# Performance work log

Hardware: AMD Instinct MI355X
Metric: run time of the kernel (lower is better)

## Reference

```python
import jax, jax.numpy as jnp
import numpy as np

GRID_H = GRID_W = 17
IMG_H = IMG_W = 128
HFOV = 60.0
ZNEAR, ZFAR = 1.0, 100.0          # FoVPerspectiveCameras defaults
Z_EPS = 0.01                      # MeshRasterizerWithZClamp.z_eps
BLUR_RADIUS = 1e-4
K_FACES = 8                       # faces_per_pixel
SIGMA = 1e-4
GAMMA = 1e-4
BG_COLOR = np.array([0.0, 0.0, 0.0], dtype=np.float32)
Z_BACKGROUND = 100.0


def _build_faces(H, W):
    # Exact replication of the 8 list comprehensions in NovelViewProjector.__init__ (flip=False)
    idx = lambda y, x: y * W + x
    f = []
    for ny in range(0, H - 1, 2):
        for nx in range(1, W - 1, 2):
            f.append([idx(ny, nx + 1), idx(ny, nx), idx(ny + 1, nx)])
    for ny in range(0, H - 1, 2):
        for nx in range(1, W - 1, 2):
            f.append([idx(ny, nx + 1), idx(ny + 1, nx), idx(ny + 1, nx + 1)])
    for ny in range(0, H - 1, 2):
        for nx in range(0, W - 1, 2):
            f.append([idx(ny, nx + 1), idx(ny, nx), idx(ny + 1, nx + 1)])
    for ny in range(0, H - 1, 2):
        for nx in range(0, W - 1, 2):
            f.append([idx(ny + 1, nx + 1), idx(ny, nx), idx(ny + 1, nx)])
    for ny in range(1, H - 1, 2):
        for nx in range(0, W - 1, 2):
            f.append([idx(ny, nx + 1), idx(ny, nx), idx(ny + 1, nx)])
    for ny in range(1, H - 1, 2):
        for nx in range(0, W - 1, 2):
            f.append([idx(ny, nx + 1), idx(ny + 1, nx), idx(ny + 1, nx + 1)])
    for ny in range(1, H - 1, 2):
        for nx in range(1, W - 1, 2):
            f.append([idx(ny, nx + 1), idx(ny, nx), idx(ny + 1, nx + 1)])
    for ny in range(1, H - 1, 2):
        for nx in range(1, W - 1, 2):
            f.append([idx(ny + 1, nx + 1), idx(ny, nx), idx(ny + 1, nx)])
    return np.array(f, dtype=np.int32)


_FACES = _build_faces(GRID_H, GRID_W)                                   # [F,3]
_xs_uv = np.linspace(1, 0, GRID_W)
_ys_uv = np.linspace(0, 1, GRID_H)
_VERTS_UVS = np.array([[x, y] for y in _ys_uv for x in _xs_uv], np.float32)  # [V,2]
_xs = np.linspace(-1, 1, GRID_W)
_ys = np.linspace(-1, 1, GRID_H)
_UNSCALED_GRID = np.array([[x, y] for y in _ys for x in _xs], np.float32)   # [V,2]
_SCALE = np.float32(np.tan(np.deg2rad(HFOV) / 2.0))                     # x_scale = y_scale


def _bilinear(tex, x, y):
    # tex [H,W,3], x/y float pixel coords [P,K] -> [P,K,3]
    H, W = tex.shape[0], tex.shape[1]
    x0f = jnp.clip(jnp.floor(x), 0, W - 1)
    y0f = jnp.clip(jnp.floor(y), 0, H - 1)
    x0 = x0f.astype(jnp.int32)
    y0 = y0f.astype(jnp.int32)
    x1 = jnp.minimum(x0 + 1, W - 1)
    y1 = jnp.minimum(y0 + 1, H - 1)
    wx = (x - x0f)[..., None]
    wy = (y - y0f)[..., None]
    top = (1 - wx) * tex[y0, x0] + wx * tex[y0, x1]
    bot = (1 - wx) * tex[y1, x0] + wx * tex[y1, x1]
    return (1 - wy) * top + wy * bot


def _rasterize_shade(verts_screen, tex):
    # verts_screen [V,3] (ndc xy, view-space z), tex [H,W,3] -> [H,W,5] RGBA+depth
    faces = jnp.asarray(_FACES)
    fv = verts_screen[faces]                 # [F,3,3]
    v2 = fv[:, :, :2]                        # screen xy per face vertex
    zf = fv[:, :, 2]                         # view-space z (z-clamped screen z)
    # pixel NDC grid, pytorch3d convention: +X left, +Y up, row 0 at top
    xs = 1.0 - 2.0 * (jnp.arange(IMG_W, dtype=jnp.float32) + 0.5) / IMG_W
    ys = 1.0 - 2.0 * (jnp.arange(IMG_H, dtype=jnp.float32) + 0.5) / IMG_H
    py, px = jnp.meshgrid(ys, xs, indexing='ij')
    pix = jnp.stack([px.reshape(-1), py.reshape(-1)], -1)       # [P,2]
    a, b, c = v2[:, 0], v2[:, 1], v2[:, 2]                      # [F,2]
    p = pix[:, None, :]                                          # [P,1,2]

    def edge(p, q, r):  # (q-p) x (r-p) -> [P,F]
        return ((q[:, 0] - p[..., 0]) * (r[:, 1] - p[..., 1])
                - (q[:, 1] - p[..., 1]) * (r[:, 0] - p[..., 0]))

    w0 = edge(p, b, c)
    w1 = edge(p, c, a)
    w2 = edge(p, a, b)
    area = (b[:, 0] - a[:, 0]) * (c[:, 1] - a[:, 1]) - (b[:, 1] - a[:, 1]) * (c[:, 0] - a[:, 0])
    area_s = jnp.where(jnp.abs(area) < 1e-8, 1e-8, area)
    bary = jnp.stack([w0, w1, w2], -1) / area_s[None, :, None]   # [P,F,3]
    inside = jnp.all(bary >= 0.0, axis=-1)
    # perspective-correct barycentrics: wi' = wi * prod(z_j, j!=i) / denom
    z0, z1, z2 = zf[:, 0], zf[:, 1], zf[:, 2]
    n0 = bary[..., 0] * z1 * z2
    n1 = bary[..., 1] * z0 * z2
    n2 = bary[..., 2] * z0 * z1
    den = n0 + n1 + n2
    den = jnp.where(jnp.abs(den) < 1e-10, 1e-10, den)
    baryp = jnp.stack([n0, n1, n2], -1) / den[..., None]
    baryc = jnp.clip(baryp, 0.0, None)                           # clip_barycentric_coords
    baryc = baryc / jnp.clip(baryc.sum(-1, keepdims=True), 1e-10, None)
    zpix = jnp.einsum('pfk,fk->pf', baryc, zf)                   # interpolated depth

    def seg_d2(p, s, e):  # squared point-to-segment distance [P,F]
        d = e - s
        t = ((p[..., 0] - s[:, 0]) * d[:, 0] + (p[..., 1] - s[:, 1]) * d[:, 1]) \
            / jnp.clip((d * d).sum(-1), 1e-12, None)
        t = jnp.clip(t, 0.0, 1.0)
        cx = s[:, 0] + t * d[:, 0]
        cy = s[:, 1] + t * d[:, 1]
        return (p[..., 0] - cx) ** 2 + (p[..., 1] - cy) ** 2

    d2 = jnp.minimum(jnp.minimum(seg_d2(p, a, b), seg_d2(p, b, c)), seg_d2(p, c, a))
    sdist = jnp.where(inside, -d2, d2)                           # signed squared dist
    valid = (sdist < BLUR_RADIUS) & (zpix > 1e-4)
    key = jnp.where(valid, zpix, jnp.inf)
    _, idxf = jax.lax.top_k(-key, K_FACES)                       # K nearest faces [P,K]
    take = lambda t: jnp.take_along_axis(t, idxf, axis=1)
    zk = take(zpix)
    dk = take(sdist)
    vk = take(valid.astype(jnp.float32))
    bk = jnp.take_along_axis(baryc, idxf[..., None], axis=1)     # [P,K,3]
    # TexturesUV sampling: interpolate uv, bilinear-sample map (v flipped)
    face_uvs = jnp.asarray(_VERTS_UVS)[faces]                    # [F,3,2]
    uvk = jnp.einsum('pkc,pkcd->pkd', bk, face_uvs[idxf])        # [P,K,2]
    tx = uvk[..., 0] * (tex.shape[1] - 1)
    ty = (1.0 - uvk[..., 1]) * (tex.shape[0] - 1)
    colors = _bilinear(tex, tx, ty)                              # [P,K,3]
    # SoftRGBDShader: softmax rgb blend + z_background depth blend
    prob = jax.nn.sigmoid(-dk / SIGMA) * vk
    alpha = 1.0 - jnp.prod(1.0 - prob, axis=-1)
    zk_s = jnp.where(vk > 0, zk, ZFAR)
    zinv = (ZFAR - zk_s) / (ZFAR - ZNEAR) * vk
    zmax = jnp.clip(zinv.max(-1, keepdims=True), 1e-10, None)
    wnum = prob * jnp.exp((zinv - zmax) / GAMMA)
    delta = jnp.exp((1e-10 - zmax) / GAMMA)                      # background weight [P,1]
    denom = wnum.sum(-1, keepdims=True) + delta
    rgb = (jnp.einsum('pk,pkc->pc', wnum, colors) + delta * jnp.asarray(BG_COLOR)) / denom
    depth = ((wnum * zk_s).sum(-1, keepdims=True) + delta * Z_BACKGROUND) / denom
    out = jnp.concatenate([rgb, alpha[:, None], depth], -1)      # [P,5]
    return out.reshape(IMG_H, IMG_W, 5)


def _forward(xy_offset, z_grid, rgb_in, R_in, T_in, R_out, T_out):
    # vertex un-projection from input view
    scaled_grid = (jnp.asarray(_UNSCALED_GRID) + xy_offset) * _SCALE      # [B,V,2]
    ones = jnp.ones(scaled_grid.shape[:-1] + (1,), scaled_grid.dtype)
    scaled_verts = jnp.concatenate([scaled_grid, ones], -1) * z_grid      # [B,V,3]
    # cam2world (inverse of pytorch3d world->view  v@R + T):  world = (view - T) @ R^T
    verts_world = jnp.einsum('bvj,bkj->bvk', scaled_verts - T_in[:, None, :], R_in)
    # output view transform + FoV perspective projection with z-clamp
    verts_view = jnp.einsum('bvj,bjk->bvk', verts_world, R_out) + T_out[:, None, :]
    s = 1.0 / _SCALE
    z = verts_view[..., 2]
    zden = jnp.where(z >= 0, jnp.maximum(z, Z_EPS), jnp.minimum(z, -Z_EPS))
    verts_screen = jnp.stack([s * verts_view[..., 0] / zden,
                              s * verts_view[..., 1] / zden, z], -1)      # [B,V,3]
    # directly_use_img_as_texture=True -> texture_image_rec = rgb_in
    images = jax.vmap(_rasterize_shade)(verts_screen, rgb_in)             # [B,H,W,5]
    return images


def setup_inputs() -> dict:
    key = jax.random.key(0)
    k1, k2, k3 = jax.random.split(key, 3)
    B, V = 1, GRID_H * GRID_W
    xy_offset = 0.01 * jax.random.normal(k1, (B, V, 2), jnp.float32)
    z_grid = 1.5 + 3.0 * jax.random.uniform(k2, (B, V, 1), jnp.float32)
    rgb_in = jax.random.uniform(k3, (B, IMG_H, IMG_W, 3), jnp.float32)
    R_in = jnp.tile(jnp.eye(3, dtype=jnp.float32)[None], (B, 1, 1))
    T_in = jnp.zeros((B, 3), jnp.float32)
    th = 0.08  # small novel-view rotation about y
    Ry = np.array([[np.cos(th), 0, np.sin(th)], [0, 1, 0], [-np.sin(th), 0, np.cos(th)]], np.float32)
    R_out = jnp.tile(jnp.asarray(Ry)[None], (B, 1, 1))
    T_out = jnp.tile(jnp.asarray(np.array([0.05, 0.0, 0.1], np.float32))[None], (B, 1))
    return {"xy_offset": xy_offset, "z_grid": z_grid, "rgb_in": rgb_in,
            "R_in": R_in, "T_in": T_in, "R_out": R_out, "T_out": T_out}


def reference(xy_offset, z_grid, rgb_in, R_in, T_in, R_out, T_out):
    # returns [B,H,W,5]: rgba = out[...,:4], depth = out[...,4]
    return _forward(xy_offset, z_grid, rgb_in, R_in, T_in, R_out, T_out)
```

## Files before the change

kernel.cpp:

```cpp
#include <hip/hip_runtime.h>
#include <math.h>

#define NVERT 289
#define NFACE 512
#define MAXB 128

__device__ __forceinline__ float frcp(float x) {
#if __has_builtin(__builtin_amdgcn_rcpf)
    return __builtin_amdgcn_rcpf(x);
#else
    return 1.0f / x;
#endif
}

__device__ __forceinline__ void face_verts(int f, int& v0, int& v1, int& v2) {
    int g = f >> 6, i = f & 63, rr = i >> 3, cc = i & 7;
    int ny = 2 * rr + (g >> 2);
    int oddx = ((g & 2) ? 0 : 1) ^ (g >> 2);
    int nx = 2 * cc + oddx;
    int p = g & 3;
    const int dy0[4] = {0, 0, 0, 1};
    const int dy1[4] = {0, 1, 0, 0};
    const int dx2[4] = {0, 1, 1, 0};
    v0 = (ny + dy0[p]) * 17 + nx + 1;
    v1 = (ny + dy1[p]) * 17 + nx;
    v2 = (ny + 1) * 17 + nx + dx2[p];
}

__global__ __launch_bounds__(512) void nvp_kernel(
    const float* __restrict__ xy_off,
    const float* __restrict__ z_grid,
    const float* __restrict__ texd,
    const float* __restrict__ R_in,
    const float* __restrict__ T_in,
    const float* __restrict__ R_out,
    const float* __restrict__ T_out,
    float* __restrict__ out)
{
    __shared__ __align__(16) float s_f[MAXB * 28];
    __shared__ float s_vx[NVERT], s_vy[NVERT], s_vz[NVERT];
    __shared__ int s_list[MAXB];
    __shared__ int s_nf;
    __shared__ int s_wcnt[8];
    __shared__ float s_tz[8][64][9];
    __shared__ unsigned char s_ti[8][64][9];
    __shared__ int   s_sel[64][9];
    __shared__ float s_zmax[64];
    __shared__ float s_pS[8][64], s_pR[8][64], s_pG[8][64];
    __shared__ float s_pB[8][64], s_pD[8][64], s_pO[8][64];

    const int tid = threadIdx.x;
    const int lane = tid & 63;
    const int wv = tid >> 6;
    const int tileX = blockIdx.x & 15;
    const int tileY = blockIdx.x >> 4;

    const float SC = 0.57735026918962576f;
    const float SI = 1.0f / 0.57735026918962576f;
    const float INF = __builtin_inff();

    if (tid < NVERT) {
        int v = tid;
        int ix = v % 17, iy = v / 17;
        float gx = -1.0f + 0.125f * (float)ix;
        float gy = -1.0f + 0.125f * (float)iy;
        float2 off = ((const float2*)xy_off)[v];
        float sx = (gx + off.x) * SC;
        float sy = (gy + off.y) * SC;
        float z = z_grid[v];
        float X = sx * z, Y = sy * z, Z = z;
        float p0 = X - T_in[0], p1 = Y - T_in[1], p2 = Z - T_in[2];
        float wxx = R_in[0] * p0 + R_in[1] * p1 + R_in[2] * p2;
        float wyy = R_in[3] * p0 + R_in[4] * p1 + R_in[5] * p2;
        float wzz = R_in[6] * p0 + R_in[7] * p1 + R_in[8] * p2;
        float vx = wxx * R_out[0] + wyy * R_out[3] + wzz * R_out[6] + T_out[0];
        float vy = wxx * R_out[1] + wyy * R_out[4] + wzz * R_out[7] + T_out[1];
        float vz = wxx * R_out[2] + wyy * R_out[5] + wzz * R_out[8] + T_out[2];
        float zden = (vz >= 0.0f) ? fmaxf(vz, 0.01f) : fminf(vz, -0.01f);
        float rz = frcp(zden);
        s_vx[v] = SI * vx * rz;
        s_vy[v] = SI * vy * rz;
        s_vz[v] = vz;
    }
    __syncthreads();

    const float pxmax = 1.0f - ((float)(tileX * 8) + 0.5f) * (1.0f / 64.0f);
    const float pxmin = 1.0f - ((float)(tileX * 8) + 7.5f) * (1.0f / 64.0f);
    const float pymax = 1.0f - ((float)(tileY * 8) + 0.5f) * (1.0f / 64.0f);
    const float pymin = 1.0f - ((float)(tileY * 8) + 7.5f) * (1.0f / 64.0f);
    const float MARG = 0.015f;

    bool ov;
    {
        int f = tid;
        int v0, v1, v2;
        face_verts(f, v0, v1, v2);
        float ax = s_vx[v0], ay = s_vy[v0];
        float bx = s_vx[v1], by = s_vy[v1];
        float cx = s_vx[v2], cy = s_vy[v2];
        float minx = fminf(ax, fminf(bx, cx)), maxx = fmaxf(ax, fmaxf(bx, cx));
        float miny = fminf(ay, fminf(by, cy)), maxy = fmaxf(ay, fmaxf(by, cy));
        ov = (minx - MARG <= pxmax) && (maxx + MARG >= pxmin) &&
             (miny - MARG <= pymax) && (maxy + MARG >= pymin);
    }
    unsigned long long wmask = __ballot(ov);
    if (lane == 0) s_wcnt[wv] = (int)__popcll(wmask);
    __syncthreads();

    {
        int base = 0, total = 0;
#pragma unroll
        for (int w = 0; w < 8; ++w) {
            int c = s_wcnt[w];
            if (w < wv) base += c;
            total += c;
        }
        if (ov) {
            int pos = base + (int)__popcll(wmask & ((1ull << lane) - 1ull));
            if (pos < MAXB) s_list[pos] = tid;
        }
        if (tid == 0) s_nf = (total < MAXB) ? total : MAXB;
    }
    __syncthreads();

    const int nf = s_nf;

    if (tid < nf) {
        int f = s_list[tid];
        int v0, v1, v2;
        face_verts(f, v0, v1, v2);
        float ax = s_vx[v0], ay = s_vy[v0], z0 = s_vz[v0];
        float bx = s_vx[v1], by = s_vy[v1], z1 = s_vz[v1];
        float cx = s_vx[v2], cy = s_vy[v2], z2 = s_vz[v2];
        float* F = &s_f[tid * 28];
        F[0] = ax; F[1] = ay; F[2] = bx; F[3] = by; F[4] = cx; F[5] = cy;
        float dabx = bx - ax, daby = by - ay;
        F[6] = dabx; F[7] = daby;
        F[8] = frcp(fmaxf(dabx * dabx + daby * daby, 1e-12f));
        float dbcx = cx - bx, dbcy = cy - by;
        F[9] = dbcx; F[10] = dbcy;
        F[11] = frcp(fmaxf(dbcx * dbcx + dbcy * dbcy, 1e-12f));
        float dcax = ax - cx, dcay = ay - cy;
        F[12] = dcax; F[13] = dcay;
        F[14] = frcp(fmaxf(dcax * dcax + dcay * dcay, 1e-12f));
        float area = dabx * (cy - ay) - daby * (cx - ax);
        float areas = (fabsf(area) < 1e-8f) ? 1e-8f : area;
        F[15] = frcp(areas);
        F[16] = z0; F[17] = z1; F[18] = z2;
        F[19] = z1 * z2; F[20] = z0 * z2; F[21] = z0 * z1;
        int ix0 = v0 % 17, iy0 = v0 / 17;
        int ix1 = v1 % 17, iy1 = v1 / 17;
        int ix2 = v2 % 17, iy2 = v2 / 17;
        F[22] = 1.0f - 0.0625f * (float)ix0; F[23] = 0.0625f * (float)iy0;
        F[24] = 1.0f - 0.0625f * (float)ix1; F[25] = 0.0625f * (float)iy1;
        F[26] = 1.0f - 0.0625f * (float)ix2; F[27] = 0.0625f * (float)iy2;
    }
    __syncthreads();

    const int p = lane;
    const int sl = wv;
    const int x = tileX * 8 + (p & 7);
    const int y = tileY * 8 + (p >> 3);
    const float px = 1.0f - ((float)x + 0.5f) * (1.0f / 64.0f);
    const float py = 1.0f - ((float)y + 0.5f) * (1.0f / 64.0f);

    float kk[8];
    int ii[8];
#pragma unroll
    for (int j = 0; j < 8; ++j) { kk[j] = INF; ii[j] = 255; }

    for (int i = sl; i < nf; i += 8) {
        const float4* Fp = (const float4*)(&s_f[i * 28]);
        const float4 f0 = Fp[0], f1 = Fp[1], f2 = Fp[2], f3 = Fp[3];
        const float ax = f0.x, ay = f0.y, bx = f0.z, by = f0.w, cx = f1.x, cy = f1.y;
        float t, ex, ey, d2;
        t = ((px - ax) * f1.z + (py - ay) * f1.w) * f2.x;
        t = fminf(fmaxf(t, 0.0f), 1.0f);
        ex = px - (ax + t * f1.z); ey = py - (ay + t * f1.w);
        d2 = ex * ex + ey * ey;
        t = ((px - bx) * f2.y + (py - by) * f2.z) * f2.w;
        t = fminf(fmaxf(t, 0.0f), 1.0f);
        ex = px - (bx + t * f2.y); ey = py - (by + t * f2.z);
        d2 = fminf(d2, ex * ex + ey * ey);
        t = ((px - cx) * f3.x + (py - cy) * f3.y) * f3.z;
        t = fminf(fmaxf(t, 0.0f), 1.0f);
        ex = px - (cx + t * f3.x); ey = py - (cy + t * f3.y);
        d2 = fminf(d2, ex * ex + ey * ey);
        float w0 = (bx - px) * (cy - py) - (by - py) * (cx - px);
        float w1 = (cx - px) * (ay - py) - (cy - py) * (ax - px);
        float w2 = (ax - px) * (by - py) - (ay - py) * (bx - px);
        float b0 = w0 * f3.w, b1 = w1 * f3.w, b2 = w2 * f3.w;
        bool inside = (b0 >= 0.0f) && (b1 >= 0.0f) && (b2 >= 0.0f);
        float sd = inside ? -d2 : d2;
        if (sd < 1e-4f) {
            const float4 f4 = Fp[4], f5 = Fp[5];
            float n0 = b0 * f4.w, n1 = b1 * f5.x, n2 = b2 * f5.y;
            float den = n0 + n1 + n2;
            den = (fabsf(den) < 1e-10f) ? 1e-10f : den;
            float iden = frcp(den);
            float c0 = fmaxf(n0 * iden, 0.0f);
            float c1 = fmaxf(n1 * iden, 0.0f);
            float c2 = fmaxf(n2 * iden, 0.0f);
            float iscn = frcp(fmaxf(c0 + c1 + c2, 1e-10f));
            float zp = (c0 * f4.x + c1 * f4.y + c2 * f4.z) * iscn;
            if (zp > 1e-4f && zp < kk[7]) {
#pragma unroll
                for (int j = 7; j >= 1; --j) {
                    bool m1 = zp < kk[j];
                    bool m2 = zp < kk[j - 1];
                    kk[j] = m1 ? (m2 ? kk[j - 1] : zp) : kk[j];
                    ii[j] = m1 ? (m2 ? ii[j - 1] : i) : ii[j];
                }
                if (zp < kk[0]) { kk[0] = zp; ii[0] = i; }
            }
        }
    }

#pragma unroll
    for (int j = 0; j < 8; ++j) {
        s_tz[sl][p][j] = kk[j];
        s_ti[sl][p][j] = (unsigned char)ii[j];
    }
    __syncthreads();

    if (tid < 64) {
        const int pp = tid;
        float z0 = s_tz[0][pp][0], z1 = s_tz[1][pp][0];
        float z2 = s_tz[2][pp][0], z3 = s_tz[3][pp][0];
        float z4 = s_tz[4][pp][0], z5 = s_tz[5][pp][0];
        float z6 = s_tz[6][pp][0], z7 = s_tz[7][pp][0];
        int h0 = 0, h1 = 0, h2 = 0, h3 = 0, h4 = 0, h5 = 0, h6 = 0, h7 = 0;
#pragma unroll
        for (int j = 0; j < 8; ++j) {
            int sA = (z1 < z0) ? 1 : 0; float zA = fminf(z0, z1);
            int sB = (z3 < z2) ? 3 : 2; float zB = fminf(z2, z3);
            int sC = (z5 < z4) ? 5 : 4; float zC = fminf(z4, z5);
            int sD = (z7 < z6) ? 7 : 6; float zD = fminf(z6, z7);
            int sAB = (zB < zA) ? sB : sA; float zAB = fminf(zA, zB);
            int sCD = (zD < zC) ? sD : sC; float zCD = fminf(zC, zD);
            int sw = (zCD < zAB) ? sCD : sAB; float zw = fminf(zAB, zCD);
            if (j == 0) s_zmax[pp] = fmaxf(1e-10f, (100.0f - zw) * (1.0f / 99.0f));
            int code = -1;
            if (zw < 3.0e38f) {
                if      (sw == 0) { code =      h0; ++h0; z0 = (h0 < 8) ? s_tz[0][pp][h0] : INF; }
                else if (sw == 1) { code = 8  | h1; ++h1; z1 = (h1 < 8) ? s_tz[1][pp][h1] : INF; }
                else if (sw == 2) { code = 16 | h2; ++h2; z2 = (h2 < 8) ? s_tz[2][pp][h2] : INF; }
                else if (sw == 3) { code = 24 | h3; ++h3; z3 = (h3 < 8) ? s_tz[3][pp][h3] : INF; }
                else if (sw == 4) { code = 32 | h4; ++h4; z4 = (h4 < 8) ? s_tz[4][pp][h4] : INF; }
                else if (sw == 5) { code = 40 | h5; ++h5; z5 = (h5 < 8) ? s_tz[5][pp][h5] : INF; }
                else if (sw == 6) { code = 48 | h6; ++h6; z6 = (h6 < 8) ? s_tz[6][pp][h6] : INF; }
                else              { code = 56 | h7; ++h7; z7 = (h7 < 8) ? s_tz[7][pp][h7] : INF; }
            }
            s_sel[pp][j] = code;
        }
    }
    __syncthreads();

    float pS = 0.0f, pR = 0.0f, pG = 0.0f, pB = 0.0f, pD = 0.0f, pO = 1.0f;
    {
        const int code = s_sel[p][sl];
        if (code >= 0) {
            const int ss = code >> 3, hh = code & 7;
            const int ci = (int)s_ti[ss][p][hh];
            const float zk = s_tz[ss][p][hh];
            const float zmx = s_zmax[p];
            const float4* Fp = (const float4*)(&s_f[ci * 28]);
            const float4 f0 = Fp[0], f1 = Fp[1], f2 = Fp[2], f3 = Fp[3];
            const float4 f4 = Fp[4], f5 = Fp[5], f6 = Fp[6];
            const float ax = f0.x, ay = f0.y, bx = f0.z, by = f0.w, cx = f1.x, cy = f1.y;
            float t, ex, ey, d2;
            t = ((px - ax) * f1.z + (py - ay) * f1.w) * f2.x;
            t = fminf(fmaxf(t, 0.0f), 1.0f);
            ex = px - (ax + t * f1.z); ey = py - (ay + t * f1.w);
            d2 = ex * ex + ey * ey;
            t = ((px - bx) * f2.y + (py - by) * f2.z) * f2.w;
            t = fminf(fmaxf(t, 0.0f), 1.0f);
            ex = px - (bx + t * f2.y); ey = py - (by + t * f2.z);
            d2 = fminf(d2, ex * ex + ey * ey);
            t = ((px - cx) * f3.x + (py - cy) * f3.y) * f3.z;
            t = fminf(fmaxf(t, 0.0f), 1.0f);
            ex = px - (cx + t * f3.x); ey = py - (cy + t * f3.y);
            d2 = fminf(d2, ex * ex + ey * ey);
            float w0 = (bx - px) * (cy - py) - (by - py) * (cx - px);
            float w1 = (cx - px) * (ay - py) - (cy - py) * (ax - px);
            float w2 = (ax - px) * (by - py) - (ay - py) * (bx - px);
            float b0 = w0 * f3.w, b1 = w1 * f3.w, b2 = w2 * f3.w;
            bool inside = (b0 >= 0.0f) && (b1 >= 0.0f) && (b2 >= 0.0f);
            float sd = inside ? -d2 : d2;
            float n0 = b0 * f4.w, n1 = b1 * f5.x, n2 = b2 * f5.y;
            float den = n0 + n1 + n2;
            den = (fabsf(den) < 1e-10f) ? 1e-10f : den;
            float iden = frcp(den);
            float c0 = fmaxf(n0 * iden, 0.0f);
            float c1 = fmaxf(n1 * iden, 0.0f);
            float c2 = fmaxf(n2 * iden, 0.0f);
            float iscn = frcp(fmaxf(c0 + c1 + c2, 1e-10f));
            float bc0 = c0 * iscn, bc1 = c1 * iscn, bc2 = c2 * iscn;
            float u = bc0 * f5.z + bc1 * f6.x + bc2 * f6.z;
            float v = bc0 * f5.w + bc1 * f6.y + bc2 * f6.w;
            float tx = u * 127.0f;
            float ty = (1.0f - v) * 127.0f;
            float x0f = fminf(fmaxf(floorf(tx), 0.0f), 127.0f);
            float y0f = fminf(fmaxf(floorf(ty), 0.0f), 127.0f);
            int x0 = (int)x0f, y0 = (int)y0f;
            int x1 = (x0 + 1 < 127) ? x0 + 1 : 127;
            int y1 = (y0 + 1 < 127) ? y0 + 1 : 127;
            float wx = tx - x0f, wy = ty - y0f;
            const float* t00 = texd + (y0 * 128 + x0) * 3;
            const float* t01 = texd + (y0 * 128 + x1) * 3;
            const float* t10 = texd + (y1 * 128 + x0) * 3;
            const float* t11 = texd + (y1 * 128 + x1) * 3;
            float r  = (1.0f - wy) * ((1.0f - wx) * t00[0] + wx * t01[0]) + wy * ((1.0f - wx) * t10[0] + wx * t11[0]);
            float gc = (1.0f - wy) * ((1.0f - wx) * t00[1] + wx * t01[1]) + wy * ((1.0f - wx) * t10[1] + wx * t11[1]);
            float bc = (1.0f - wy) * ((1.0f - wx) * t00[2] + wx * t01[2]) + wy * ((1.0f - wx) * t10[2] + wx * t11[2]);
            float prob = frcp(1.0f + __expf(sd * 1e4f));
            float zi = (100.0f - zk) * (1.0f / 99.0f);
            float wgt = prob * __expf((zi - zmx) * 1e4f);
            pS = wgt; pR = wgt * r; pG = wgt * gc; pB = wgt * bc; pD = wgt * zk;
            pO = 1.0f - prob;
        }
    }
    s_pS[sl][p] = pS; s_pR[sl][p] = pR; s_pG[sl][p] = pG;
    s_pB[sl][p] = pB; s_pD[sl][p] = pD; s_pO[sl][p] = pO;
    __syncthreads();

    if (tid < 64) {
        float S = 0.0f, aR = 0.0f, aG = 0.0f, aB = 0.0f, aD = 0.0f, om = 1.0f;
#pragma unroll
        for (int w = 0; w < 8; ++w) {
            S  += s_pS[w][tid];
            aR += s_pR[w][tid];
            aG += s_pG[w][tid];
            aB += s_pB[w][tid];
            aD += s_pD[w][tid];
            om *= s_pO[w][tid];
        }
        float delta = __expf((1e-10f - s_zmax[tid]) * 1e4f);
        S += delta;
        aD += delta * 100.0f;
        float invS = frcp(S);
        const int o = (y * 128 + x) * 5;
        out[o + 0] = aR * invS;
        out[o + 1] = aG * invS;
        out[o + 2] = aB * invS;
        out[o + 3] = 1.0f - om;
        out[o + 4] = aD * invS;
    }
}

extern "C" void kernel_launch(void* const* d_in, const int* in_sizes, int n_in,
                              void* d_out, int out_size, void* d_ws, size_t ws_size,
                              hipStream_t stream) {
    const float* xy_off = (const float*)d_in[0];
    const float* zg     = (const float*)d_in[1];
    const float* rgb    = (const float*)d_in[2];
    const float* R_in   = (const float*)d_in[3];
    const float* T_in   = (const float*)d_in[4];
    const float* R_out  = (const float*)d_in[5];
    const float* T_out  = (const float*)d_in[6];
    float* out = (float*)d_out;
    nvp_kernel<<<dim3(256), dim3(512), 0, stream>>>(xy_off, zg, rgb, R_in, T_in,
                                                    R_out, T_out, out);
}
```

Measured before the change: 72.03 us.

## Move per-pixel face slices into 8-lane groups and merge with shuffles

Pixel-to-thread mapping changes so the 8 face slices of one pixel sit in adjacent lanes of one wavefront, not spread across 8 wavefronts. The k-way top-8 merge, the final accumulation and the output write now use width-8 cross-lane shuffles, replacing shared-memory staging and three block barriers. Face setup is folded into the compaction step, which drops the index list and another barrier. In exchange each pixel's merge runs 8 rounds of butterfly shuffles with register shifts, which adds ALU work per lane.

```diff
diff --git a/kernel.cpp b/kernel.cpp
--- a/kernel.cpp
+++ b/kernel.cpp
@@ -39,15 +39,8 @@
 {
     __shared__ __align__(16) float s_f[MAXB * 28];
     __shared__ float s_vx[NVERT], s_vy[NVERT], s_vz[NVERT];
-    __shared__ int s_list[MAXB];
+    __shared__ int s_wcnt[8];
     __shared__ int s_nf;
-    __shared__ int s_wcnt[8];
-    __shared__ float s_tz[8][64][9];
-    __shared__ unsigned char s_ti[8][64][9];
-    __shared__ int   s_sel[64][9];
-    __shared__ float s_zmax[64];
-    __shared__ float s_pS[8][64], s_pR[8][64], s_pG[8][64];
-    __shared__ float s_pB[8][64], s_pD[8][64], s_pO[8][64];
 
     const int tid = threadIdx.x;
     const int lane = tid & 63;
@@ -115,50 +108,47 @@
             if (w < wv) base += c;
             total += c;
         }
+        if (tid == 0) s_nf = (total < MAXB) ? total : MAXB;
         if (ov) {
             int pos = base + (int)__popcll(wmask & ((1ull << lane) - 1ull));
-            if (pos < MAXB) s_list[pos] = tid;
-        }
-        if (tid == 0) s_nf = (total < MAXB) ? total : MAXB;
+            if (pos < MAXB) {
+                int f = tid;
+                int v0, v1, v2;
+                face_verts(f, v0, v1, v2);
+                float ax = s_vx[v0], ay = s_vy[v0], z0 = s_vz[v0];
+                float bx = s_vx[v1], by = s_vy[v1], z1 = s_vz[v1];
+                float cx = s_vx[v2], cy = s_vy[v2], z2 = s_vz[v2];
+                float* F = &s_f[pos * 28];
+                F[0] = ax; F[1] = ay; F[2] = bx; F[3] = by; F[4] = cx; F[5] = cy;
+                float dabx = bx - ax, daby = by - ay;
+                F[6] = dabx; F[7] = daby;
+                F[8] = frcp(fmaxf(dabx * dabx + daby * daby, 1e-12f));
+                float dbcx = cx - bx, dbcy = cy - by;
+                F[9] = dbcx; F[10] = dbcy;
+                F[11] = frcp(fmaxf(dbcx * dbcx + dbcy * dbcy, 1e-12f));
+                float dcax = ax - cx, dcay = ay - cy;
+                F[12] = dcax; F[13] = dcay;
+                F[14] = frcp(fmaxf(dcax * dcax + dcay * dcay, 1e-12f));
+                float area = dabx * (cy - ay) - daby * (cx - ax);
+                float areas = (fabsf(area) < 1e-8f) ? 1e-8f : area;
+                F[15] = frcp(areas);
+                F[16] = z0; F[17] = z1; F[18] = z2;
+                F[19] = z1 * z2; F[20] = z0 * z2; F[21] = z0 * z1;
+                int ix0 = v0 % 17, iy0 = v0 / 17;
+                int ix1 = v1 % 17, iy1 = v1 / 17;
+                int ix2 = v2 % 17, iy2 = v2 / 17;
+                F[22] = 1.0f - 0.0625f * (float)ix0; F[23] = 0.0625f * (float)iy0;
+                F[24] = 1.0f - 0.0625f * (float)ix1; F[25] = 0.0625f * (float)iy1;
+                F[26] = 1.0f - 0.0625f * (float)ix2; F[27] = 0.0625f * (float)iy2;
+            }
+        }
     }
     __syncthreads();
 
     const int nf = s_nf;
 
-    if (tid < nf) {
-        int f = s_list[tid];
-        int v0, v1, v2;
-        face_verts(f, v0, v1, v2);
-        float ax = s_vx[v0], ay = s_vy[v0], z0 = s_vz[v0];
-        float bx = s_vx[v1], by = s_vy[v1], z1 = s_vz[v1];
-        float cx = s_vx[v2], cy = s_vy[v2], z2 = s_vz[v2];
-        float* F = &s_f[tid * 28];
-        F[0] = ax; F[1] = ay; F[2] = bx; F[3] = by; F[4] = cx; F[5] = cy;
-        float dabx = bx - ax, daby = by - ay;
-        F[6] = dabx; F[7] = daby;
-        F[8] = frcp(fmaxf(dabx * dabx + daby * daby, 1e-12f));
-        float dbcx = cx - bx, dbcy = cy - by;
-        F[9] = dbcx; F[10] = dbcy;
-        F[11] = frcp(fmaxf(dbcx * dbcx + dbcy * dbcy, 1e-12f));
-        float dcax = ax - cx, dcay = ay - cy;
-        F[12] = dcax; F[13] = dcay;
-        F[14] = frcp(fmaxf(dcax * dcax + dcay * dcay, 1e-12f));
-        float area = dabx * (cy - ay) - daby * (cx - ax);
-        float areas = (fabsf(area) < 1e-8f) ? 1e-8f : area;
-        F[15] = frcp(areas);
-        F[16] = z0; F[17] = z1; F[18] = z2;
-        F[19] = z1 * z2; F[20] = z0 * z2; F[21] = z0 * z1;
-        int ix0 = v0 % 17, iy0 = v0 / 17;
-        int ix1 = v1 % 17, iy1 = v1 / 17;
-        int ix2 = v2 % 17, iy2 = v2 / 17;
-        F[22] = 1.0f - 0.0625f * (float)ix0; F[23] = 0.0625f * (float)iy0;
-        F[24] = 1.0f - 0.0625f * (float)ix1; F[25] = 0.0625f * (float)iy1;
-        F[26] = 1.0f - 0.0625f * (float)ix2; F[27] = 0.0625f * (float)iy2;
-    }
-    __syncthreads();
-
-    const int p = lane;
-    const int sl = wv;
+    const int l = tid & 7;
+    const int p = tid >> 3;
     const int x = tileX * 8 + (p & 7);
     const int y = tileY * 8 + (p >> 3);
     const float px = 1.0f - ((float)x + 0.5f) * (1.0f / 64.0f);
@@ -167,9 +157,9 @@
     float kk[8];
     int ii[8];
 #pragma unroll
-    for (int j = 0; j < 8; ++j) { kk[j] = INF; ii[j] = 255; }
-
-    for (int i = sl; i < nf; i += 8) {
+    for (int j = 0; j < 8; ++j) { kk[j] = INF; ii[j] = -1; }
+
+    for (int i = l; i < nf; i += 8) {
         const float4* Fp = (const float4*)(&s_f[i * 28]);
         const float4 f0 = Fp[0], f1 = Fp[1], f2 = Fp[2], f3 = Fp[3];
         const float ax = f0.x, ay = f0.y, bx = f0.z, by = f0.w, cx = f1.x, cy = f1.y;
@@ -216,136 +206,119 @@
         }
     }
 
+    float hz = kk[0];
+    int hf = ii[0];
+    float selz = INF;
+    int self_ = -1;
+    float zfirst = INF;
 #pragma unroll
     for (int j = 0; j < 8; ++j) {
-        s_tz[sl][p][j] = kk[j];
-        s_ti[sl][p][j] = (unsigned char)ii[j];
-    }
-    __syncthreads();
-
-    if (tid < 64) {
-        const int pp = tid;
-        float z0 = s_tz[0][pp][0], z1 = s_tz[1][pp][0];
-        float z2 = s_tz[2][pp][0], z3 = s_tz[3][pp][0];
-        float z4 = s_tz[4][pp][0], z5 = s_tz[5][pp][0];
-        float z6 = s_tz[6][pp][0], z7 = s_tz[7][pp][0];
-        int h0 = 0, h1 = 0, h2 = 0, h3 = 0, h4 = 0, h5 = 0, h6 = 0, h7 = 0;
-#pragma unroll
-        for (int j = 0; j < 8; ++j) {
-            int sA = (z1 < z0) ? 1 : 0; float zA = fminf(z0, z1);
-            int sB = (z3 < z2) ? 3 : 2; float zB = fminf(z2, z3);
-            int sC = (z5 < z4) ? 5 : 4; float zC = fminf(z4, z5);
-            int sD = (z7 < z6) ? 7 : 6; float zD = fminf(z6, z7);
-            int sAB = (zB < zA) ? sB : sA; float zAB = fminf(zA, zB);
-            int sCD = (zD < zC) ? sD : sC; float zCD = fminf(zC, zD);
-            int sw = (zCD < zAB) ? sCD : sAB; float zw = fminf(zAB, zCD);
-            if (j == 0) s_zmax[pp] = fmaxf(1e-10f, (100.0f - zw) * (1.0f / 99.0f));
-            int code = -1;
-            if (zw < 3.0e38f) {
-                if      (sw == 0) { code =      h0; ++h0; z0 = (h0 < 8) ? s_tz[0][pp][h0] : INF; }
-                else if (sw == 1) { code = 8  | h1; ++h1; z1 = (h1 < 8) ? s_tz[1][pp][h1] : INF; }
-                else if (sw == 2) { code = 16 | h2; ++h2; z2 = (h2 < 8) ? s_tz[2][pp][h2] : INF; }
-                else if (sw == 3) { code = 24 | h3; ++h3; z3 = (h3 < 8) ? s_tz[3][pp][h3] : INF; }
-                else if (sw == 4) { code = 32 | h4; ++h4; z4 = (h4 < 8) ? s_tz[4][pp][h4] : INF; }
-                else if (sw == 5) { code = 40 | h5; ++h5; z5 = (h5 < 8) ? s_tz[5][pp][h5] : INF; }
-                else if (sw == 6) { code = 48 | h6; ++h6; z6 = (h6 < 8) ? s_tz[6][pp][h6] : INF; }
-                else              { code = 56 | h7; ++h7; z7 = (h7 < 8) ? s_tz[7][pp][h7] : INF; }
-            }
-            s_sel[pp][j] = code;
-        }
-    }
-    __syncthreads();
+        float mz = hz;
+        int ml = l;
+#pragma unroll
+        for (int m = 1; m < 8; m <<= 1) {
+            float oz = __shfl_xor(mz, m, 8);
+            int ol = __shfl_xor(ml, m, 8);
+            bool take = (oz < mz) || ((oz == mz) && (ol < ml));
+            mz = take ? oz : mz;
+            ml = take ? ol : ml;
+        }
+        int wf = __shfl(hf, ml, 8);
+        if (j == 0) zfirst = mz;
+        if (l == j) { selz = mz; self_ = wf; }
+        if (ml == l) {
+#pragma unroll
+            for (int q = 0; q < 7; ++q) { kk[q] = kk[q + 1]; ii[q] = ii[q + 1]; }
+            kk[7] = INF; ii[7] = -1;
+            hz = kk[0]; hf = ii[0];
+        }
+    }
+    const float zmx = fmaxf(1e-10f, (100.0f - zfirst) * (1.0f / 99.0f));
 
     float pS = 0.0f, pR = 0.0f, pG = 0.0f, pB = 0.0f, pD = 0.0f, pO = 1.0f;
-    {
-        const int code = s_sel[p][sl];
-        if (code >= 0) {
-            const int ss = code >> 3, hh = code & 7;
-            const int ci = (int)s_ti[ss][p][hh];
-            const float zk = s_tz[ss][p][hh];
-            const float zmx = s_zmax[p];
-            const float4* Fp = (const float4*)(&s_f[ci * 28]);
-            const float4 f0 = Fp[0], f1 = Fp[1], f2 = Fp[2], f3 = Fp[3];
-            const float4 f4 = Fp[4], f5 = Fp[5], f6 = Fp[6];
-            const float ax = f0.x, ay = f0.y, bx = f0.z, by = f0.w, cx = f1.x, cy = f1.y;
-            float t, ex, ey, d2;
-            t = ((px - ax) * f1.z + (py - ay) * f1.w) * f2.x;
-            t = fminf(fmaxf(t, 0.0f), 1.0f);
-            ex = px - (ax + t * f1.z); ey = py - (ay + t * f1.w);
-            d2 = ex * ex + ey * ey;
-            t = ((px - bx) * f2.y + (py - by) * f2.z) * f2.w;
-            t = fminf(fmaxf(t, 0.0f), 1.0f);
-            ex = px - (bx + t * f2.y); ey = py - (by + t * f2.z);
-            d2 = fminf(d2, ex * ex + ey * ey);
-            t = ((px - cx) * f3.x + (py - cy) * f3.y) * f3.z;
-            t = fminf(fmaxf(t, 0.0f), 1.0f);
-            ex = px - (cx + t * f3.x); ey = py - (cy + t * f3.y);
-            d2 = fminf(d2, ex * ex + ey * ey);
-            float w0 = (bx - px) * (cy - py) - (by - py) * (cx - px);
-            float w1 = (cx - px) * (ay - py) - (cy - py) * (ax - px);
-            float w2 = (ax - px) * (by - py) - (ay - py) * (bx - px);
-            float b0 = w0 * f3.w, b1 = w1 * f3.w, b2 = w2 * f3.w;
-            bool inside = (b0 >= 0.0f) && (b1 >= 0.0f) && (b2 >= 0.0f);
-            float sd = inside ? -d2 : d2;
-            float n0 = b0 * f4.w, n1 = b1 * f5.x, n2 = b2 * f5.y;
-            float den = n0 + n1 + n2;
-            den = (fabsf(den) < 1e-10f) ? 1e-10f : den;
-            float iden = frcp(den);
-            float c0 = fmaxf(n0 * iden, 0.0f);
-            float c1 = fmaxf(n1 * iden, 0.0f);
-            float c2 = fmaxf(n2 * iden, 0.0f);
-            float iscn = frcp(fmaxf(c0 + c1 + c2, 1e-10f));
-            float bc0 = c0 * iscn, bc1 = c1 * iscn, bc2 = c2 * iscn;
-            float u = bc0 * f5.z + bc1 * f6.x + bc2 * f6.z;
-            float v = bc0 * f5.w + bc1 * f6.y + bc2 * f6.w;
-            float tx = u * 127.0f;
-            float ty = (1.0f - v) * 127.0f;
-            float x0f = fminf(fmaxf(floorf(tx), 0.0f), 127.0f);
-            float y0f = fminf(fmaxf(floorf(ty), 0.0f), 127.0f);
-            int x0 = (int)x0f, y0 = (int)y0f;
-            int x1 = (x0 + 1 < 127) ? x0 + 1 : 127;
-            int y1 = (y0 + 1 < 127) ? y0 + 1 : 127;
-            float wx = tx - x0f, wy = ty - y0f;
-            const float* t00 = texd + (y0 * 128 + x0) * 3;
-            const float* t01 = texd + (y0 * 128 + x1) * 3;
-            const float* t10 = texd + (y1 * 128 + x0) * 3;
-            const float* t11 = texd + (y1 * 128 + x1) * 3;
-            float r  = (1.0f - wy) * ((1.0f - wx) * t00[0] + wx * t01[0]) + wy * ((1.0f - wx) * t10[0] + wx * t11[0]);
-            float gc = (1.0f - wy) * ((1.0f - wx) * t00[1] + wx * t01[1]) + wy * ((1.0f - wx) * t10[1] + wx * t11[1]);
-            float bc = (1.0f - wy) * ((1.0f - wx) * t00[2] + wx * t01[2]) + wy * ((1.0f - wx) * t10[2] + wx * t11[2]);
-            float prob = frcp(1.0f + __expf(sd * 1e4f));
-            float zi = (100.0f - zk) * (1.0f / 99.0f);
-            float wgt = prob * __expf((zi - zmx) * 1e4f);
-            pS = wgt; pR = wgt * r; pG = wgt * gc; pB = wgt * bc; pD = wgt * zk;
-            pO = 1.0f - prob;
-        }
-    }
-    s_pS[sl][p] = pS; s_pR[sl][p] = pR; s_pG[sl][p] = pG;
-    s_pB[sl][p] = pB; s_pD[sl][p] = pD; s_pO[sl][p] = pO;
-    __syncthreads();
-
-    if (tid < 64) {
-        float S = 0.0f, aR = 0.0f, aG = 0.0f, aB = 0.0f, aD = 0.0f, om = 1.0f;
-#pragma unroll
-        for (int w = 0; w < 8; ++w) {
-            S  += s_pS[w][tid];
-            aR += s_pR[w][tid];
-            aG += s_pG[w][tid];
-            aB += s_pB[w][tid];
-            aD += s_pD[w][tid];
-            om *= s_pO[w][tid];
-        }
-        float delta = __expf((1e-10f - s_zmax[tid]) * 1e4f);
-        S += delta;
-        aD += delta * 100.0f;
-        float invS = frcp(S);
-        const int o = (y * 128 + x) * 5;
-        out[o + 0] = aR * invS;
-        out[o + 1] = aG * invS;
-        out[o + 2] = aB * invS;
-        out[o + 3] = 1.0f - om;
-        out[o + 4] = aD * invS;
-    }
+    if (selz < 3.0e38f) {
+        const int ci = self_;
+        const float zk = selz;
+        const float4* Fp = (const float4*)(&s_f[ci * 28]);
+        const float4 f0 = Fp[0], f1 = Fp[1], f2 = Fp[2], f3 = Fp[3];
+        const float4 f4 = Fp[4], f5 = Fp[5], f6 = Fp[6];
+        const float ax = f0.x, ay = f0.y, bx = f0.z, by = f0.w, cx = f1.x, cy = f1.y;
+        float t, ex, ey, d2;
+        t = ((px - ax) * f1.z + (py - ay) * f1.w) * f2.x;
+        t = fminf(fmaxf(t, 0.0f), 1.0f);
+        ex = px - (ax + t * f1.z); ey = py - (ay + t * f1.w);
+        d2 = ex * ex + ey * ey;
+        t = ((px - bx) * f2.y + (py - by) * f2.z) * f2.w;
+        t = fminf(fmaxf(t, 0.0f), 1.0f);
+        ex = px - (bx + t * f2.y); ey = py - (by + t * f2.z);
+        d2 = fminf(d2, ex * ex + ey * ey);
+        t = ((px - cx) * f3.x + (py - cy) * f3.y) * f3.z;
+        t = fminf(fmaxf(t, 0.0f), 1.0f);
+        ex = px - (cx + t * f3.x); ey = py - (cy + t * f3.y);
+        d2 = fminf(d2, ex * ex + ey * ey);
+        float w0 = (bx - px) * (cy - py) - (by - py) * (cx - px);
+        float w1 = (cx - px) * (ay - py) - (cy - py) * (ax - px);
+        float w2 = (ax - px) * (by - py) - (ay - py) * (bx - px);
+        float b0 = w0 * f3.w, b1 = w1 * f3.w, b2 = w2 * f3.w;
+        bool inside = (b0 >= 0.0f) && (b1 >= 0.0f) && (b2 >= 0.0f);
+        float sd = inside ? -d2 : d2;
+        float n0 = b0 * f4.w, n1 = b1 * f5.x, n2 = b2 * f5.y;
+        float den = n0 + n1 + n2;
+        den = (fabsf(den) < 1e-10f) ? 1e-10f : den;
+        float iden = frcp(den);
+        float c0 = fmaxf(n0 * iden, 0.0f);
+        float c1 = fmaxf(n1 * iden, 0.0f);
+        float c2 = fmaxf(n2 * iden, 0.0f);
+        float iscn = frcp(fmaxf(c0 + c1 + c2, 1e-10f));
+        float bc0 = c0 * iscn, bc1 = c1 * iscn, bc2 = c2 * iscn;
+        float u = bc0 * f5.z + bc1 * f6.x + bc2 * f6.z;
+        float v = bc0 * f5.w + bc1 * f6.y + bc2 * f6.w;
+        float tx = u * 127.0f;
+        float ty = (1.0f - v) * 127.0f;
+        float x0f = fminf(fmaxf(floorf(tx), 0.0f), 127.0f);
+        float y0f = fminf(fmaxf(floorf(ty), 0.0f), 127.0f);
+        int x0 = (int)x0f, y0 = (int)y0f;
+        int x1 = (x0 + 1 < 127) ? x0 + 1 : 127;
+        int y1 = (y0 + 1 < 127) ? y0 + 1 : 127;
+        float wx = tx - x0f, wy = ty - y0f;
+        const float* t00 = texd + (y0 * 128 + x0) * 3;
+        const float* t01 = texd + (y0 * 128 + x1) * 3;
+        const float* t10 = texd + (y1 * 128 + x0) * 3;
+        const float* t11 = texd + (y1 * 128 + x1) * 3;
+        float r  = (1.0f - wy) * ((1.0f - wx) * t00[0] + wx * t01[0]) + wy * ((1.0f - wx) * t10[0] + wx * t11[0]);
+        float gc = (1.0f - wy) * ((1.0f - wx) * t00[1] + wx * t01[1]) + wy * ((1.0f - wx) * t10[1] + wx * t11[1]);
+        float bc = (1.0f - wy) * ((1.0f - wx) * t00[2] + wx * t01[2]) + wy * ((1.0f - wx) * t10[2] + wx * t11[2]);
+        float prob = frcp(1.0f + __expf(sd * 1e4f));
+        float zi = (100.0f - zk) * (1.0f / 99.0f);
+        float wgt = prob * __expf((zi - zmx) * 1e4f);
+        pS = wgt; pR = wgt * r; pG = wgt * gc; pB = wgt * bc; pD = wgt * zk;
+        pO = 1.0f - prob;
+    }
+
+#pragma unroll
+    for (int m = 1; m < 8; m <<= 1) {
+        pS += __shfl_xor(pS, m, 8);
+        pR += __shfl_xor(pR, m, 8);
+        pG += __shfl_xor(pG, m, 8);
+        pB += __shfl_xor(pB, m, 8);
+        pD += __shfl_xor(pD, m, 8);
+        pO *= __shfl_xor(pO, m, 8);
+    }
+    float delta = __expf((1e-10f - zmx) * 1e4f);
+    float S = pS + delta;
+    float invS = frcp(S);
+    float v0 = pR * invS;
+    float v1 = pG * invS;
+    float v2 = pB * invS;
+    float v3 = 1.0f - pO;
+    float v4 = (pD + delta * 100.0f) * invS;
+    float val = v0;
+    val = (l == 1) ? v1 : val;
+    val = (l == 2) ? v2 : val;
+    val = (l == 3) ? v3 : val;
+    val = (l == 4) ? v4 : val;
+    const int o = (y * 128 + x) * 5;
+    if (l < 5) out[o + l] = val;
 }
 
 extern "C" void kernel_launch(void* const* d_in, const int* in_sizes, int n_in,
```

New measurement: 71.83 us. Within noise of the previous version (-0.3%).
